# Kernel tuning notes

Hardware: AMD Instinct MI355X
Metric: run time of the kernel (lower is better)

The kernel has to match this reference:

```python
import jax, jax.numpy as jnp
import numpy as np


def setup_inputs() -> dict:
    key = jax.random.key(0)
    ks = jax.random.split(key, 12)
    B, S, D = 2, 1024, 1024       # batch, seq_len, hidden
    DF_S, DF_E, E = 2048, 512, 8   # shared ffn, expert ffn, n_experts
    W = 0.02                       # weight init scale
    x = jax.random.normal(ks[0], (B, S, D), jnp.float32)
    router_weight = jax.random.normal(ks[1], (E, D), jnp.float32) * W
    sh_gate_w = jax.random.normal(ks[2], (DF_S, D), jnp.float32) * W
    sh_up_w = jax.random.normal(ks[3], (DF_S, D), jnp.float32) * W
    sh_down_w = jax.random.normal(ks[4], (D, DF_S), jnp.float32) * W
    gate_q = jax.random.randint(ks[5], (E, DF_E, D), -128, 128, jnp.int32)
    up_q = jax.random.randint(ks[6], (E, DF_E, D), -128, 128, jnp.int32)
    down_q = jax.random.randint(ks[7], (E, D, DF_E), -128, 128, jnp.int32)
    gate_s = jax.random.uniform(ks[8], (E, DF_E), jnp.float32) * 0.001
    up_s = jax.random.uniform(ks[9], (E, DF_E), jnp.float32) * 0.001
    down_s = jax.random.uniform(ks[10], (E, D), jnp.float32) * 0.001
    alpha = 0.5 + jax.random.uniform(ks[11], (E,), jnp.float32)  # effective_alpha per expert
    return dict(x=x, router_weight=router_weight, sh_gate_w=sh_gate_w,
                sh_up_w=sh_up_w, sh_down_w=sh_down_w, gate_s=gate_s,
                up_s=up_s, down_s=down_s, alpha=alpha, gate_q=gate_q,
                up_q=up_q, down_q=down_q, top_k=2)


def reference(x, router_weight, sh_gate_w, sh_up_w, sh_down_w,
              gate_s, up_s, down_s, alpha, gate_q, up_q, down_q, top_k):
    B, S, D = x.shape
    T = B * S
    E = router_weight.shape[0]
    xf = x.reshape(T, D).astype(jnp.float32)
    # shared SwiGLU MLP
    shared = (jax.nn.silu(xf @ sh_gate_w.T) * (xf @ sh_up_w.T)) @ sh_down_w.T  # [T, D]
    # router: top-k + softmax over selected logits
    logits = xf @ router_weight.T                                # [T, E]
    k = min(int(top_k), E)
    vals, idx = jax.lax.top_k(logits, k)
    w = jax.nn.softmax(vals, axis=-1)                            # [T, k]
    # scatter routing weights into dense combine matrix [T, E] (topk idx are distinct)
    combine = jnp.zeros((T, E), jnp.float32).at[jnp.arange(T)[:, None], idx].add(w)
    # on-the-fly dequantization: int8-range quants * per-row scale
    gw = gate_q.astype(jnp.float32) * gate_s[..., None]          # [E, DF_E, D]
    uw = up_q.astype(jnp.float32) * up_s[..., None]              # [E, DF_E, D]
    dw = down_q.astype(jnp.float32) * down_s[..., None]          # [E, D, DF_E]
    # expert SwiGLU for every (token, expert) pair, combined by routing weights
    g = jnp.einsum('td,efd->tef', xf, gw)                        # [T, E, DF_E]
    u = jnp.einsum('td,efd->tef', xf, uw)
    eo = jnp.einsum('tef,edf->ted', jax.nn.silu(g) * u, dw)      # [T, E, D]
    delta = eo - shared[:, None, :]                              # expert output minus shared
    mixed = shared + jnp.einsum('te,ted->td', combine * alpha[None, :], delta)
    return mixed.reshape(B, S, D)
```

## Files before the change

### kernel.cpp

```cpp
#include <hip/hip_runtime.h>
#include <math.h>

#define T_TOK 2048
#define D_DIM 1024
#define E_NUM 8
#define DFS   2048
#define DFE   512

#define BM 64
#define BN 64
#define BK 32

typedef short short8 __attribute__((ext_vector_type(8)));
typedef float floatx4 __attribute__((ext_vector_type(4)));
typedef unsigned short ushort;

__device__ __forceinline__ ushort f2b(float f) {
  union { float f; unsigned u; } v; v.f = f;
  unsigned r = (v.u + 0x7fffu + ((v.u >> 16) & 1u)) >> 16;
  return (ushort)r;
}

__device__ __forceinline__ void gld16(const ushort* g, ushort* l) {
  __builtin_amdgcn_global_load_lds(
      (const __attribute__((address_space(1))) void*)g,
      (__attribute__((address_space(3))) void*)l,
      16, 0, 0);
}

__device__ __forceinline__ float silu_mul(float g, float u) {
  return (g / (1.f + __expf(-g))) * u;
}

__global__ __launch_bounds__(256) void mega_prep(
    const float* __restrict__ x, const float* __restrict__ rw,
    const float* __restrict__ alpha,
    const float* __restrict__ sg, const float* __restrict__ su,
    const float* __restrict__ sd,
    const int* __restrict__ gq, const int* __restrict__ uq,
    const int* __restrict__ dq,
    int* __restrict__ choice, float2* __restrict__ cpair,
    float* __restrict__ csum, ushort* __restrict__ xb,
    ushort* __restrict__ sgb, ushort* __restrict__ subb,
    ushort* __restrict__ sdb,
    ushort* __restrict__ gqb, ushort* __restrict__ uqb,
    ushort* __restrict__ dqb) {
  const int b = blockIdx.x;
  const int tid = threadIdx.x;
  if (b < 512) {
    __shared__ float xs[4 * D_DIM];
    const size_t base = (size_t)b * 4 * D_DIM;
#pragma unroll
    for (int j = 0; j < 4; ++j) {
      const int idx = j * 1024 + tid * 4;
      float4 v = *(const float4*)(x + base + idx);
      *(float4*)&xs[idx] = v;
      union { ushort u[4]; uint2 p; } o;
      o.u[0] = f2b(v.x); o.u[1] = f2b(v.y); o.u[2] = f2b(v.z); o.u[3] = f2b(v.w);
      *(uint2*)(xb + base + idx) = o.p;
    }
    __syncthreads();
    const int w = tid >> 6, l = tid & 63;
    const int t = b * 4 + w;
    const int e = l >> 3, sub = l & 7;
    const float* wr = rw + e * D_DIM;
    float acc = 0.f;
#pragma unroll
    for (int k = 0; k < 32; ++k) {
      const int d = k * 32 + sub * 4;
      float4 xv = *(const float4*)&xs[w * D_DIM + d];
      float4 wv = *(const float4*)(wr + d);
      acc += xv.x * wv.x + xv.y * wv.y + xv.z * wv.z + xv.w * wv.w;
    }
    acc += __shfl_xor(acc, 1);
    acc += __shfl_xor(acc, 2);
    acc += __shfl_xor(acc, 4);
    float lg[8];
#pragma unroll
    for (int i = 0; i < 8; ++i) lg[i] = __shfl(acc, i * 8);
    if (l == 0) {
      int i0 = 0; float v0 = lg[0];
#pragma unroll
      for (int i = 1; i < E_NUM; ++i) if (lg[i] > v0) { v0 = lg[i]; i0 = i; }
      int i1 = -1; float v1 = -1e30f;
#pragma unroll
      for (int i = 0; i < E_NUM; ++i) {
        if (i == i0) continue;
        if (lg[i] > v1) { v1 = lg[i]; i1 = i; }
      }
      float w0 = 1.f / (1.f + __expf(v1 - v0));
      float w1 = 1.f - w0;
      float c0 = w0 * alpha[i0];
      float c1 = w1 * alpha[i1];
      csum[t] = c0 + c1;
      choice[t] = i0 | (i1 << 4);
      cpair[t] = make_float2(c0, c1);
    }
  } else if (b < 512 + 3072) {
    const int bb = b - 512;
    const int which = bb >> 10;
    const float* src; ushort* dst;
    if (which == 0) { src = sg; dst = sgb; }
    else if (which == 1) { src = su; dst = subb; }
    else { src = sd; dst = sdb; }
    const size_t i = (size_t)(bb & 1023) * 256 + tid;
    const float4* sp = (const float4*)src;
    float4 a = sp[2 * i], c = sp[2 * i + 1];
    union { ushort u[8]; uint4 v; } o;
    o.u[0] = f2b(a.x); o.u[1] = f2b(a.y); o.u[2] = f2b(a.z); o.u[3] = f2b(a.w);
    o.u[4] = f2b(c.x); o.u[5] = f2b(c.y); o.u[6] = f2b(c.z); o.u[7] = f2b(c.w);
    ((uint4*)dst)[i] = o.v;
  } else {
    const int bb = b - 3584;
    const int which = bb >> 11;
    const int* src; ushort* dst;
    if (which == 0) { src = gq; dst = gqb; }
    else if (which == 1) { src = uq; dst = uqb; }
    else { src = dq; dst = dqb; }
    const size_t i = (size_t)(bb & 2047) * 256 + tid;
    const int4* sp = (const int4*)src;
    int4 a = sp[2 * i], c = sp[2 * i + 1];
    union { ushort u[8]; uint4 v; } o;
    o.u[0] = f2b((float)a.x); o.u[1] = f2b((float)a.y);
    o.u[2] = f2b((float)a.z); o.u[3] = f2b((float)a.w);
    o.u[4] = f2b((float)c.x); o.u[5] = f2b((float)c.y);
    o.u[6] = f2b((float)c.z); o.u[7] = f2b((float)c.w);
    ((uint4*)dst)[i] = o.v;
  }
}

__global__ __launch_bounds__(1024) void build_lists(
    const int* __restrict__ choice, int* __restrict__ cnt,
    int* __restrict__ tok_list, uint2* __restrict__ ass) {
  __shared__ int lcnt[E_NUM];
  __shared__ int lbase[E_NUM];
  const int tid = threadIdx.x;
  if (tid < E_NUM) lcnt[tid] = 0;
  __syncthreads();
  uint2 tmp[T_TOK / 1024];
#pragma unroll
  for (int r = 0; r < T_TOK / 1024; ++r) {
    const int t = r * 1024 + tid;
    const int ch = choice[t];
    const int i0 = ch & 15, i1 = ch >> 4;
    const int p0 = atomicAdd(&lcnt[i0], 1);
    tok_list[i0 * T_TOK + p0] = t;
    const int p1 = atomicAdd(&lcnt[i1], 1);
    tok_list[i1 * T_TOK + p1] = t;
    tmp[r] = make_uint2((unsigned)((i0 << 16) | p0), (unsigned)((i1 << 16) | p1));
  }
  __syncthreads();
  if (tid < E_NUM) {
    int b = 0;
    for (int i = 0; i < tid; ++i) b += lcnt[i];
    lbase[tid] = b;
    cnt[tid] = lcnt[tid];
    cnt[8 + tid] = b;
  }
  __syncthreads();
#pragma unroll
  for (int r = 0; r < T_TOK / 1024; ++r) {
    const int t = r * 1024 + tid;
    const uint2 v = tmp[r];
    ass[t] = make_uint2(lbase[v.x >> 16] + (v.x & 0xffffu),
                        lbase[v.y >> 16] + (v.y & 0xffffu));
  }
}


__global__ __launch_bounds__(256) void mfma_shared_gateup(
    const ushort* __restrict__ xb, const ushort* __restrict__ wg,
    const ushort* __restrict__ wu, ushort* __restrict__ sbuf) {
  __shared__ ushort As[BM * BK];
  __shared__ ushort Bg[BN * BK];
  __shared__ ushort Bu[BN * BK];
  const int tid = threadIdx.x;
  const int wave = tid >> 6, lane = tid & 63;
  const int wr = wave >> 1, wc = wave & 1;
  const int m0 = blockIdx.y * BM, n0 = blockIdx.x * BN;
  const int srow = lane >> 2;
  const int scol = (lane & 3) * 8;
  const int K = D_DIM;

  const ushort* a0 = xb + (size_t)(m0 + wave * 16 + srow) * K + scol;
  const ushort* g0 = wg + (size_t)(n0 + wave * 16 + srow) * K + scol;
  const ushort* u0 = wu + (size_t)(n0 + wave * 16 + srow) * K + scol;
  ushort* lA0 = &As[(wave * 16) * BK];
  ushort* lG0 = &Bg[(wave * 16) * BK];
  ushort* lU0 = &Bu[(wave * 16) * BK];

  floatx4 accg[2][2], accu[2][2];
#pragma unroll
  for (int i = 0; i < 2; ++i)
#pragma unroll
    for (int j = 0; j < 2; ++j) { accg[i][j] = (floatx4)(0.f); accu[i][j] = (floatx4)(0.f); }

  const int kc = (lane >> 4) * 8;
  const int rb = lane & 15;

  for (int k0 = 0; k0 < K; k0 += BK) {
    gld16(a0 + k0, lA0);
    gld16(g0 + k0, lG0);
    gld16(u0 + k0, lU0);
    __syncthreads();
    short8 af[2], gf[2], uf[2];
#pragma unroll
    for (int mt = 0; mt < 2; ++mt)
      af[mt] = *(const short8*)&As[(wr * 32 + mt * 16 + rb) * BK + kc];
#pragma unroll
    for (int nt = 0; nt < 2; ++nt) {
      gf[nt] = *(const short8*)&Bg[(wc * 32 + nt * 16 + rb) * BK + kc];
      uf[nt] = *(const short8*)&Bu[(wc * 32 + nt * 16 + rb) * BK + kc];
    }
#pragma unroll
    for (int mt = 0; mt < 2; ++mt)
#pragma unroll
      for (int nt = 0; nt < 2; ++nt) {
        accg[mt][nt] = __builtin_amdgcn_mfma_f32_16x16x32_bf16(af[mt], gf[nt], accg[mt][nt], 0, 0, 0);
        accu[mt][nt] = __builtin_amdgcn_mfma_f32_16x16x32_bf16(af[mt], uf[nt], accu[mt][nt], 0, 0, 0);
      }
    __syncthreads();
  }
#pragma unroll
  for (int mt = 0; mt < 2; ++mt)
#pragma unroll
    for (int nt = 0; nt < 2; ++nt) {
      const int col = n0 + wc * 32 + nt * 16 + rb;
#pragma unroll
      for (int r = 0; r < 4; ++r) {
        const int row = m0 + wr * 32 + mt * 16 + (lane >> 4) * 4 + r;
        float s = silu_mul(accg[mt][nt][r], accu[mt][nt][r]);
        sbuf[(size_t)row * DFS + col] = f2b(s);
      }
    }
}

__global__ __launch_bounds__(256) void mfma_shared_down(
    const ushort* __restrict__ sb, const ushort* __restrict__ wd,
    float* __restrict__ shd0, float* __restrict__ shd1) {
  __shared__ ushort As[BM * BK];
  __shared__ ushort Bs[BN * BK];
  const int tid = threadIdx.x;
  const int wave = tid >> 6, lane = tid & 63;
  const int wr = wave >> 1, wc = wave & 1;
  const int m0 = blockIdx.y * BM, n0 = blockIdx.x * BN;
  const int kb = blockIdx.z * (DFS / 2);
  float* dst = blockIdx.z ? shd1 : shd0;
  const int srow = lane >> 2;
  const int scol = (lane & 3) * 8;

  const ushort* a0 = sb + (size_t)(m0 + wave * 16 + srow) * DFS + kb + scol;
  const ushort* b0 = wd + (size_t)(n0 + wave * 16 + srow) * DFS + kb + scol;
  ushort* lA0 = &As[(wave * 16) * BK];
  ushort* lB0 = &Bs[(wave * 16) * BK];

  floatx4 acc[2][2];
#pragma unroll
  for (int i = 0; i < 2; ++i)
#pragma unroll
    for (int j = 0; j < 2; ++j) acc[i][j] = (floatx4)(0.f);

  const int kc = (lane >> 4) * 8;
  const int rb = lane & 15;

  for (int k0 = 0; k0 < DFS / 2; k0 += BK) {
    gld16(a0 + k0, lA0);
    gld16(b0 + k0, lB0);
    __syncthreads();
    short8 af[2], bf[2];
#pragma unroll
    for (int mt = 0; mt < 2; ++mt)
      af[mt] = *(const short8*)&As[(wr * 32 + mt * 16 + rb) * BK + kc];
#pragma unroll
    for (int nt = 0; nt < 2; ++nt)
      bf[nt] = *(const short8*)&Bs[(wc * 32 + nt * 16 + rb) * BK + kc];
#pragma unroll
    for (int mt = 0; mt < 2; ++mt)
#pragma unroll
      for (int nt = 0; nt < 2; ++nt)
        acc[mt][nt] = __builtin_amdgcn_mfma_f32_16x16x32_bf16(af[mt], bf[nt], acc[mt][nt], 0, 0, 0);
    __syncthreads();
  }
#pragma unroll
  for (int mt = 0; mt < 2; ++mt)
#pragma unroll
    for (int nt = 0; nt < 2; ++nt) {
      const int col = n0 + wc * 32 + nt * 16 + rb;
#pragma unroll
      for (int r = 0; r < 4; ++r) {
        const int row = m0 + wr * 32 + mt * 16 + (lane >> 4) * 4 + r;
        dst[(size_t)row * D_DIM + col] = acc[mt][nt][r];
      }
    }
}

__global__ __launch_bounds__(256) void mfma_expert_gateup(
    const ushort* __restrict__ xb, const ushort* __restrict__ gq,
    const ushort* __restrict__ uq, const float* __restrict__ gate_s,
    const float* __restrict__ up_s, const int* __restrict__ cnt,
    const int* __restrict__ tok_list, ushort* __restrict__ act) {
  const int e = blockIdx.z;
  const int ce = cnt[e];
  const int m0 = blockIdx.y * BM;
  if (m0 >= ce) return;
  const int ebase = cnt[8 + e];
  const int n0 = blockIdx.x * BN;
  __shared__ ushort As[BM * BK];
  __shared__ ushort Bg[BN * BK];
  __shared__ ushort Bu[BN * BK];
  const int tid = threadIdx.x;
  const int wave = tid >> 6, lane = tid & 63;
  const int wr = wave >> 1, wc = wave & 1;
  const int srow = lane >> 2;
  const int scol = (lane & 3) * 8;
  const int K = D_DIM;

  const int r0 = m0 + wave * 16 + srow;
  const int tk0 = (r0 < ce) ? tok_list[e * T_TOK + r0] : 0;
  const ushort* a0 = xb + (size_t)tk0 * K + scol;
  const ushort* g0 = gq + (size_t)e * DFE * D_DIM + (size_t)(n0 + wave * 16 + srow) * K + scol;
  const ushort* u0 = uq + (size_t)e * DFE * D_DIM + (size_t)(n0 + wave * 16 + srow) * K + scol;
  ushort* lA0 = &As[(wave * 16) * BK];
  ushort* lG0 = &Bg[(wave * 16) * BK];
  ushort* lU0 = &Bu[(wave * 16) * BK];

  floatx4 accg[2][2], accu[2][2];
#pragma unroll
  for (int i = 0; i < 2; ++i)
#pragma unroll
    for (int j = 0; j < 2; ++j) { accg[i][j] = (floatx4)(0.f); accu[i][j] = (floatx4)(0.f); }

  const int kc = (lane >> 4) * 8;
  const int rb = lane & 15;

  for (int k0 = 0; k0 < K; k0 += BK) {
    gld16(a0 + k0, lA0);
    gld16(g0 + k0, lG0);
    gld16(u0 + k0, lU0);
    __syncthreads();
    short8 af[2], gf[2], uf[2];
#pragma unroll
    for (int mt = 0; mt < 2; ++mt)
      af[mt] = *(const short8*)&As[(wr * 32 + mt * 16 + rb) * BK + kc];
#pragma unroll
    for (int nt = 0; nt < 2; ++nt) {
      gf[nt] = *(const short8*)&Bg[(wc * 32 + nt * 16 + rb) * BK + kc];
      uf[nt] = *(const short8*)&Bu[(wc * 32 + nt * 16 + rb) * BK + kc];
    }
#pragma unroll
    for (int mt = 0; mt < 2; ++mt)
#pragma unroll
      for (int nt = 0; nt < 2; ++nt) {
        accg[mt][nt] = __builtin_amdgcn_mfma_f32_16x16x32_bf16(af[mt], gf[nt], accg[mt][nt], 0, 0, 0);
        accu[mt][nt] = __builtin_amdgcn_mfma_f32_16x16x32_bf16(af[mt], uf[nt], accu[mt][nt], 0, 0, 0);
      }
    __syncthreads();
  }
#pragma unroll
  for (int mt = 0; mt < 2; ++mt)
#pragma unroll
    for (int nt = 0; nt < 2; ++nt) {
      const int col = n0 + wc * 32 + nt * 16 + rb;
      const float gsc = gate_s[e * DFE + col];
      const float usc = up_s[e * DFE + col];
#pragma unroll
      for (int r = 0; r < 4; ++r) {
        const int slot = m0 + wr * 32 + mt * 16 + (lane >> 4) * 4 + r;
        if (slot < ce) {
          float s = silu_mul(accg[mt][nt][r] * gsc, accu[mt][nt][r] * usc);
          act[(size_t)(ebase + slot) * DFE + col] = f2b(s);
        }
      }
    }
}

__global__ __launch_bounds__(256) void mfma_expert_down(
    const ushort* __restrict__ act, const ushort* __restrict__ dq,
    const float* __restrict__ down_s, const int* __restrict__ cnt,
    float* __restrict__ pbuf) {
  const int e = blockIdx.z;
  const int ce = cnt[e];
  const int m0 = blockIdx.y * BM;
  if (m0 >= ce) return;
  const int ebase = cnt[8 + e];
  const int n0 = blockIdx.x * BN;
  __shared__ ushort As[BM * BK];
  __shared__ ushort Bs[BN * BK];
  const int tid = threadIdx.x;
  const int wave = tid >> 6, lane = tid & 63;
  const int wr = wave >> 1, wc = wave & 1;
  const int srow = lane >> 2;
  const int scol = (lane & 3) * 8;

  const ushort* a0 = act + (size_t)(ebase + m0 + wave * 16 + srow) * DFE + scol;
  const ushort* b0 = dq + (size_t)e * D_DIM * DFE + (size_t)(n0 + wave * 16 + srow) * DFE + scol;
  ushort* lA0 = &As[(wave * 16) * BK];
  ushort* lB0 = &Bs[(wave * 16) * BK];

  floatx4 acc[2][2];
#pragma unroll
  for (int i = 0; i < 2; ++i)
#pragma unroll
    for (int j = 0; j < 2; ++j) acc[i][j] = (floatx4)(0.f);

  const int kc = (lane >> 4) * 8;
  const int rb = lane & 15;

  for (int k0 = 0; k0 < DFE; k0 += BK) {
    gld16(a0 + k0, lA0);
    gld16(b0 + k0, lB0);
    __syncthreads();
    short8 af[2], bf[2];
#pragma unroll
    for (int mt = 0; mt < 2; ++mt)
      af[mt] = *(const short8*)&As[(wr * 32 + mt * 16 + rb) * BK + kc];
#pragma unroll
    for (int nt = 0; nt < 2; ++nt)
      bf[nt] = *(const short8*)&Bs[(wc * 32 + nt * 16 + rb) * BK + kc];
#pragma unroll
    for (int mt = 0; mt < 2; ++mt)
#pragma unroll
      for (int nt = 0; nt < 2; ++nt)
        acc[mt][nt] = __builtin_amdgcn_mfma_f32_16x16x32_bf16(af[mt], bf[nt], acc[mt][nt], 0, 0, 0);
    __syncthreads();
  }
#pragma unroll
  for (int mt = 0; mt < 2; ++mt)
#pragma unroll
    for (int nt = 0; nt < 2; ++nt) {
      const int col = n0 + wc * 32 + nt * 16 + rb;
      const float dsc = down_s[e * D_DIM + col];
#pragma unroll
      for (int r = 0; r < 4; ++r) {
        const int slot = m0 + wr * 32 + mt * 16 + (lane >> 4) * 4 + r;
        if (slot < ce)
          pbuf[(size_t)(ebase + slot) * D_DIM + col] = acc[mt][nt][r] * dsc;
      }
    }
}

__global__ __launch_bounds__(256) void combine_kernel(
    const float* __restrict__ shd0, const float* __restrict__ shd1,
    const float* __restrict__ pbuf, const float* __restrict__ csum,
    const float2* __restrict__ cpair, const uint2* __restrict__ ass,
    float* __restrict__ out) {
  const int t = blockIdx.x;
  const int c4 = threadIdx.x * 4;
  const float cs = 1.f - csum[t];
  const float2 cp = cpair[t];
  const uint2 a = ass[t];
  const size_t idx = (size_t)t * D_DIM + c4;
  float4 s0 = *(const float4*)(shd0 + idx);
  float4 s1 = *(const float4*)(shd1 + idx);
  float4 e0 = *(const float4*)(pbuf + (size_t)a.x * D_DIM + c4);
  float4 e1 = *(const float4*)(pbuf + (size_t)a.y * D_DIM + c4);
  float4 o;
  o.x = cs * (s0.x + s1.x) + cp.x * e0.x + cp.y * e1.x;
  o.y = cs * (s0.y + s1.y) + cp.x * e0.y + cp.y * e1.y;
  o.z = cs * (s0.z + s1.z) + cp.x * e0.z + cp.y * e1.z;
  o.w = cs * (s0.w + s1.w) + cp.x * e0.w + cp.y * e1.w;
  *(float4*)(out + idx) = o;
}

extern "C" void kernel_launch(void* const* d_in, const int* in_sizes, int n_in,
                              void* d_out, int out_size, void* d_ws, size_t ws_size,
                              hipStream_t stream) {
  const float* x         = (const float*)d_in[0];
  const float* rw        = (const float*)d_in[1];
  const float* sh_gate_w = (const float*)d_in[2];
  const float* sh_up_w   = (const float*)d_in[3];
  const float* sh_down_w = (const float*)d_in[4];
  const float* gate_s    = (const float*)d_in[5];
  const float* up_s      = (const float*)d_in[6];
  const float* down_s    = (const float*)d_in[7];
  const float* alpha     = (const float*)d_in[8];
  const int*   gate_q    = (const int*)d_in[9];
  const int*   up_q      = (const int*)d_in[10];
  const int*   down_q    = (const int*)d_in[11];

  char* ws = (char*)d_ws;
  const size_t MB = 1u << 20;
  int*    cnt      = (int*)ws;
  int*    tok_list = (int*)(ws + 1024);
  float*  csum     = (float*)(ws + 66560);
  int*    choice   = (int*)(ws + 74752);
  float2* cpair    = (float2*)(ws + 82944);
  uint2*  ass      = (uint2*)(ws + 99328);
  ushort* xb      = (ushort*)(ws + 1 * MB);
  ushort* sgb     = (ushort*)(ws + 5 * MB);
  ushort* sub     = (ushort*)(ws + 9 * MB);
  float*  shd0    = (float*)(ws + 5 * MB);
  ushort* sbuf    = (ushort*)(ws + 13 * MB);
  ushort* sdb     = (ushort*)(ws + 21 * MB);
  ushort* gqb     = (ushort*)(ws + 25 * MB);
  ushort* uqb     = (ushort*)(ws + 33 * MB);
  float*  pbuf    = (float*)(ws + 25 * MB);
  ushort* dqb     = (ushort*)(ws + 41 * MB);
  ushort* act     = (ushort*)(ws + 49 * MB);
  float*  shd1    = (float*)(ws + 53 * MB);

  float* out = (float*)d_out;

  mega_prep<<<9728, 256, 0, stream>>>(
      x, rw, alpha, sh_gate_w, sh_up_w, sh_down_w, gate_q, up_q, down_q,
      choice, cpair, csum, xb, sgb, sub, sdb, gqb, uqb, dqb);
  build_lists<<<1, 1024, 0, stream>>>(choice, cnt, tok_list, ass);

  mfma_shared_gateup<<<dim3(DFS / BN, T_TOK / BM), 256, 0, stream>>>(xb, sgb, sub, sbuf);
  mfma_expert_gateup<<<dim3(DFE / BN, T_TOK / BM, E_NUM), 256, 0, stream>>>(
      xb, gqb, uqb, gate_s, up_s, cnt, tok_list, act);
  mfma_shared_down<<<dim3(D_DIM / BN, T_TOK / BM, 2), 256, 0, stream>>>(sbuf, sdb, shd0, shd1);
  mfma_expert_down<<<dim3(D_DIM / BN, T_TOK / BM, E_NUM), 256, 0, stream>>>(
      act, dqb, down_s, cnt, pbuf);
  combine_kernel<<<T_TOK, 256, 0, stream>>>(shd0, shd1, pbuf, csum, cpair, ass, out);
}
```

Measured before the change: 248.8 us.

## Load MFMA operands directly from global memory, dropping LDS staging and barriers

All four GEMM kernels now read their MFMA fragments straight from global memory into registers. This removes the global_load_lds staging and the two __syncthreads per K step, and the K loop is unrolled by four so loads from several iterations can be in flight together. The cost is that tiles are no longer shared through LDS: each wave refetches A and B rows that other waves in the block also read. This relies on L1/L2 caching to absorb the duplicated traffic and raises register pressure.

```diff
diff --git a/kernel.cpp b/kernel.cpp
--- a/kernel.cpp
+++ b/kernel.cpp
@@ -19,13 +19,6 @@
   union { float f; unsigned u; } v; v.f = f;
   unsigned r = (v.u + 0x7fffu + ((v.u >> 16) & 1u)) >> 16;
   return (ushort)r;
-}
-
-__device__ __forceinline__ void gld16(const ushort* g, ushort* l) {
-  __builtin_amdgcn_global_load_lds(
-      (const __attribute__((address_space(1))) void*)g,
-      (__attribute__((address_space(3))) void*)l,
-      16, 0, 0);
 }
 
 __device__ __forceinline__ float silu_mul(float g, float u) {
@@ -171,23 +164,20 @@
 __global__ __launch_bounds__(256) void mfma_shared_gateup(
     const ushort* __restrict__ xb, const ushort* __restrict__ wg,
     const ushort* __restrict__ wu, ushort* __restrict__ sbuf) {
-  __shared__ ushort As[BM * BK];
-  __shared__ ushort Bg[BN * BK];
-  __shared__ ushort Bu[BN * BK];
   const int tid = threadIdx.x;
   const int wave = tid >> 6, lane = tid & 63;
   const int wr = wave >> 1, wc = wave & 1;
   const int m0 = blockIdx.y * BM, n0 = blockIdx.x * BN;
-  const int srow = lane >> 2;
-  const int scol = (lane & 3) * 8;
+  const int rb = lane & 15;
+  const int kc = (lane >> 4) * 8;
   const int K = D_DIM;
 
-  const ushort* a0 = xb + (size_t)(m0 + wave * 16 + srow) * K + scol;
-  const ushort* g0 = wg + (size_t)(n0 + wave * 16 + srow) * K + scol;
-  const ushort* u0 = wu + (size_t)(n0 + wave * 16 + srow) * K + scol;
-  ushort* lA0 = &As[(wave * 16) * BK];
-  ushort* lG0 = &Bg[(wave * 16) * BK];
-  ushort* lU0 = &Bu[(wave * 16) * BK];
+  const ushort* ar0 = xb + (size_t)(m0 + wr * 32 + rb) * K + kc;
+  const ushort* ar1 = ar0 + (size_t)16 * K;
+  const ushort* gr0 = wg + (size_t)(n0 + wc * 32 + rb) * K + kc;
+  const ushort* gr1 = gr0 + (size_t)16 * K;
+  const ushort* ur0 = wu + (size_t)(n0 + wc * 32 + rb) * K + kc;
+  const ushort* ur1 = ur0 + (size_t)16 * K;
 
   floatx4 accg[2][2], accu[2][2];
 #pragma unroll
@@ -195,23 +185,15 @@
 #pragma unroll
     for (int j = 0; j < 2; ++j) { accg[i][j] = (floatx4)(0.f); accu[i][j] = (floatx4)(0.f); }
 
-  const int kc = (lane >> 4) * 8;
-  const int rb = lane & 15;
-
+#pragma unroll 4
   for (int k0 = 0; k0 < K; k0 += BK) {
-    gld16(a0 + k0, lA0);
-    gld16(g0 + k0, lG0);
-    gld16(u0 + k0, lU0);
-    __syncthreads();
     short8 af[2], gf[2], uf[2];
-#pragma unroll
-    for (int mt = 0; mt < 2; ++mt)
-      af[mt] = *(const short8*)&As[(wr * 32 + mt * 16 + rb) * BK + kc];
-#pragma unroll
-    for (int nt = 0; nt < 2; ++nt) {
-      gf[nt] = *(const short8*)&Bg[(wc * 32 + nt * 16 + rb) * BK + kc];
-      uf[nt] = *(const short8*)&Bu[(wc * 32 + nt * 16 + rb) * BK + kc];
-    }
+    af[0] = *(const short8*)(ar0 + k0);
+    af[1] = *(const short8*)(ar1 + k0);
+    gf[0] = *(const short8*)(gr0 + k0);
+    gf[1] = *(const short8*)(gr1 + k0);
+    uf[0] = *(const short8*)(ur0 + k0);
+    uf[1] = *(const short8*)(ur1 + k0);
 #pragma unroll
     for (int mt = 0; mt < 2; ++mt)
 #pragma unroll
@@ -219,7 +201,6 @@
         accg[mt][nt] = __builtin_amdgcn_mfma_f32_16x16x32_bf16(af[mt], gf[nt], accg[mt][nt], 0, 0, 0);
         accu[mt][nt] = __builtin_amdgcn_mfma_f32_16x16x32_bf16(af[mt], uf[nt], accu[mt][nt], 0, 0, 0);
       }
-    __syncthreads();
   }
 #pragma unroll
   for (int mt = 0; mt < 2; ++mt)
@@ -238,21 +219,19 @@
 __global__ __launch_bounds__(256) void mfma_shared_down(
     const ushort* __restrict__ sb, const ushort* __restrict__ wd,
     float* __restrict__ shd0, float* __restrict__ shd1) {
-  __shared__ ushort As[BM * BK];
-  __shared__ ushort Bs[BN * BK];
   const int tid = threadIdx.x;
   const int wave = tid >> 6, lane = tid & 63;
   const int wr = wave >> 1, wc = wave & 1;
   const int m0 = blockIdx.y * BM, n0 = blockIdx.x * BN;
   const int kb = blockIdx.z * (DFS / 2);
   float* dst = blockIdx.z ? shd1 : shd0;
-  const int srow = lane >> 2;
-  const int scol = (lane & 3) * 8;
-
-  const ushort* a0 = sb + (size_t)(m0 + wave * 16 + srow) * DFS + kb + scol;
-  const ushort* b0 = wd + (size_t)(n0 + wave * 16 + srow) * DFS + kb + scol;
-  ushort* lA0 = &As[(wave * 16) * BK];
-  ushort* lB0 = &Bs[(wave * 16) * BK];
+  const int rb = lane & 15;
+  const int kc = (lane >> 4) * 8;
+
+  const ushort* ar0 = sb + (size_t)(m0 + wr * 32 + rb) * DFS + kb + kc;
+  const ushort* ar1 = ar0 + (size_t)16 * DFS;
+  const ushort* br0 = wd + (size_t)(n0 + wc * 32 + rb) * DFS + kb + kc;
+  const ushort* br1 = br0 + (size_t)16 * DFS;
 
   floatx4 acc[2][2];
 #pragma unroll
@@ -260,26 +239,18 @@
 #pragma unroll
     for (int j = 0; j < 2; ++j) acc[i][j] = (floatx4)(0.f);
 
-  const int kc = (lane >> 4) * 8;
-  const int rb = lane & 15;
-
+#pragma unroll 4
   for (int k0 = 0; k0 < DFS / 2; k0 += BK) {
-    gld16(a0 + k0, lA0);
-    gld16(b0 + k0, lB0);
-    __syncthreads();
     short8 af[2], bf[2];
-#pragma unroll
-    for (int mt = 0; mt < 2; ++mt)
-      af[mt] = *(const short8*)&As[(wr * 32 + mt * 16 + rb) * BK + kc];
-#pragma unroll
-    for (int nt = 0; nt < 2; ++nt)
-      bf[nt] = *(const short8*)&Bs[(wc * 32 + nt * 16 + rb) * BK + kc];
+    af[0] = *(const short8*)(ar0 + k0);
+    af[1] = *(const short8*)(ar1 + k0);
+    bf[0] = *(const short8*)(br0 + k0);
+    bf[1] = *(const short8*)(br1 + k0);
 #pragma unroll
     for (int mt = 0; mt < 2; ++mt)
 #pragma unroll
       for (int nt = 0; nt < 2; ++nt)
         acc[mt][nt] = __builtin_amdgcn_mfma_f32_16x16x32_bf16(af[mt], bf[nt], acc[mt][nt], 0, 0, 0);
-    __syncthreads();
   }
 #pragma unroll
   for (int mt = 0; mt < 2; ++mt)
@@ -305,24 +276,25 @@
   if (m0 >= ce) return;
   const int ebase = cnt[8 + e];
   const int n0 = blockIdx.x * BN;
-  __shared__ ushort As[BM * BK];
-  __shared__ ushort Bg[BN * BK];
-  __shared__ ushort Bu[BN * BK];
   const int tid = threadIdx.x;
   const int wave = tid >> 6, lane = tid & 63;
   const int wr = wave >> 1, wc = wave & 1;
-  const int srow = lane >> 2;
-  const int scol = (lane & 3) * 8;
+  const int rb = lane & 15;
+  const int kc = (lane >> 4) * 8;
   const int K = D_DIM;
 
-  const int r0 = m0 + wave * 16 + srow;
+  const int r0 = m0 + wr * 32 + rb;
+  const int r1 = r0 + 16;
   const int tk0 = (r0 < ce) ? tok_list[e * T_TOK + r0] : 0;
-  const ushort* a0 = xb + (size_t)tk0 * K + scol;
-  const ushort* g0 = gq + (size_t)e * DFE * D_DIM + (size_t)(n0 + wave * 16 + srow) * K + scol;
-  const ushort* u0 = uq + (size_t)e * DFE * D_DIM + (size_t)(n0 + wave * 16 + srow) * K + scol;
-  ushort* lA0 = &As[(wave * 16) * BK];
-  ushort* lG0 = &Bg[(wave * 16) * BK];
-  ushort* lU0 = &Bu[(wave * 16) * BK];
+  const int tk1 = (r1 < ce) ? tok_list[e * T_TOK + r1] : 0;
+  const ushort* ar0 = xb + (size_t)tk0 * K + kc;
+  const ushort* ar1 = xb + (size_t)tk1 * K + kc;
+  const ushort* gqe = gq + (size_t)e * DFE * D_DIM;
+  const ushort* uqe = uq + (size_t)e * DFE * D_DIM;
+  const ushort* gr0 = gqe + (size_t)(n0 + wc * 32 + rb) * K + kc;
+  const ushort* gr1 = gr0 + (size_t)16 * K;
+  const ushort* ur0 = uqe + (size_t)(n0 + wc * 32 + rb) * K + kc;
+  const ushort* ur1 = ur0 + (size_t)16 * K;
 
   floatx4 accg[2][2], accu[2][2];
 #pragma unroll
@@ -330,23 +302,15 @@
 #pragma unroll
     for (int j = 0; j < 2; ++j) { accg[i][j] = (floatx4)(0.f); accu[i][j] = (floatx4)(0.f); }
 
-  const int kc = (lane >> 4) * 8;
-  const int rb = lane & 15;
-
+#pragma unroll 4
   for (int k0 = 0; k0 < K; k0 += BK) {
-    gld16(a0 + k0, lA0);
-    gld16(g0 + k0, lG0);
-    gld16(u0 + k0, lU0);
-    __syncthreads();
     short8 af[2], gf[2], uf[2];
-#pragma unroll
-    for (int mt = 0; mt < 2; ++mt)
-      af[mt] = *(const short8*)&As[(wr * 32 + mt * 16 + rb) * BK + kc];
-#pragma unroll
-    for (int nt = 0; nt < 2; ++nt) {
-      gf[nt] = *(const short8*)&Bg[(wc * 32 + nt * 16 + rb) * BK + kc];
-      uf[nt] = *(const short8*)&Bu[(wc * 32 + nt * 16 + rb) * BK + kc];
-    }
+    af[0] = *(const short8*)(ar0 + k0);
+    af[1] = *(const short8*)(ar1 + k0);
+    gf[0] = *(const short8*)(gr0 + k0);
+    gf[1] = *(const short8*)(gr1 + k0);
+    uf[0] = *(const short8*)(ur0 + k0);
+    uf[1] = *(const short8*)(ur1 + k0);
 #pragma unroll
     for (int mt = 0; mt < 2; ++mt)
 #pragma unroll
@@ -354,7 +318,6 @@
         accg[mt][nt] = __builtin_amdgcn_mfma_f32_16x16x32_bf16(af[mt], gf[nt], accg[mt][nt], 0, 0, 0);
         accu[mt][nt] = __builtin_amdgcn_mfma_f32_16x16x32_bf16(af[mt], uf[nt], accu[mt][nt], 0, 0, 0);
       }
-    __syncthreads();
   }
 #pragma unroll
   for (int mt = 0; mt < 2; ++mt)
@@ -384,18 +347,16 @@
   if (m0 >= ce) return;
   const int ebase = cnt[8 + e];
   const int n0 = blockIdx.x * BN;
-  __shared__ ushort As[BM * BK];
-  __shared__ ushort Bs[BN * BK];
   const int tid = threadIdx.x;
   const int wave = tid >> 6, lane = tid & 63;
   const int wr = wave >> 1, wc = wave & 1;
-  const int srow = lane >> 2;
-  const int scol = (lane & 3) * 8;
-
-  const ushort* a0 = act + (size_t)(ebase + m0 + wave * 16 + srow) * DFE + scol;
-  const ushort* b0 = dq + (size_t)e * D_DIM * DFE + (size_t)(n0 + wave * 16 + srow) * DFE + scol;
-  ushort* lA0 = &As[(wave * 16) * BK];
-  ushort* lB0 = &Bs[(wave * 16) * BK];
+  const int rb = lane & 15;
+  const int kc = (lane >> 4) * 8;
+
+  const ushort* ar0 = act + (size_t)(ebase + m0 + wr * 32 + rb) * DFE + kc;
+  const ushort* ar1 = ar0 + (size_t)16 * DFE;
+  const ushort* br0 = dq + (size_t)e * D_DIM * DFE + (size_t)(n0 + wc * 32 + rb) * DFE + kc;
+  const ushort* br1 = br0 + (size_t)16 * DFE;
 
   floatx4 acc[2][2];
 #pragma unroll
@@ -403,26 +364,18 @@
 #pragma unroll
     for (int j = 0; j < 2; ++j) acc[i][j] = (floatx4)(0.f);
 
-  const int kc = (lane >> 4) * 8;
-  const int rb = lane & 15;
-
+#pragma unroll 4
   for (int k0 = 0; k0 < DFE; k0 += BK) {
-    gld16(a0 + k0, lA0);
-    gld16(b0 + k0, lB0);
-    __syncthreads();
     short8 af[2], bf[2];
-#pragma unroll
-    for (int mt = 0; mt < 2; ++mt)
-      af[mt] = *(const short8*)&As[(wr * 32 + mt * 16 + rb) * BK + kc];
-#pragma unroll
-    for (int nt = 0; nt < 2; ++nt)
-      bf[nt] = *(const short8*)&Bs[(wc * 32 + nt * 16 + rb) * BK + kc];
+    af[0] = *(const short8*)(ar0 + k0);
+    af[1] = *(const short8*)(ar1 + k0);
+    bf[0] = *(const short8*)(br0 + k0);
+    bf[1] = *(const short8*)(br1 + k0);
 #pragma unroll
     for (int mt = 0; mt < 2; ++mt)
 #pragma unroll
       for (int nt = 0; nt < 2; ++nt)
         acc[mt][nt] = __builtin_amdgcn_mfma_f32_16x16x32_bf16(af[mt], bf[nt], acc[mt][nt], 0, 0, 0);
-    __syncthreads();
   }
 #pragma unroll
   for (int mt = 0; mt < 2; ++mt)
```

New measurement: 446.5 us. 1.79x slower.
